# Kernel tuning notes

Measured on AMD Instinct MI355X. Metric: run time of the kernel, lower is better.

Reference implementation:

```python
import jax, jax.numpy as jnp
import numpy as np

B, H, KVH, D, HID = 32, 32, 8, 128, 4096
TPB, MB = 64, 32            # tokens per block, max blocks per seq
NB = B * MB                 # cache pool blocks
S = MB * TPB                # max context = 2048
BASE = 10000.0


def setup_inputs() -> dict:
    key = jax.random.key(0)
    ks = jax.random.split(key, 10)
    ri = lambda k, sh: jax.random.randint(k, sh, -127, 128, dtype=jnp.int8)
    ru = lambda k, sh: jax.random.uniform(k, sh, minval=0.005, maxval=0.02, dtype=jnp.float32)
    return {
        'hidden_q': ri(ks[0], (B, HID)).astype(jnp.int32),
        'hidden_scale': ru(ks[1], (B,)),
        'qkv_w': ri(ks[2], ((H + 2 * KVH) * D, HID)),
        'qkv_wscale': ru(ks[3], ((H + 2 * KVH) * D,)),
        'o_w': ri(ks[4], (HID, H * D)),
        'o_wscale': ru(ks[5], (HID,)),
        'kv_cache': ri(ks[6], (NB, 2, KVH, TPB, D)),
        'kv_scale': ru(ks[7], (NB, 2, KVH, TPB)),
        'block_tables': jnp.arange(NB, dtype=jnp.int32).reshape(B, MB),
        'context_lens': jax.random.randint(ks[8], (B,), 64, S - 1, dtype=jnp.int32),
    }


def _rope_neox(x, pos):
    # x: [B, nH, D], pos: [B] -- GPT-NeoX style rotation on (first half, second half)
    half = D // 2
    inv_freq = jnp.power(BASE, -jnp.arange(half, dtype=jnp.float32) / half)
    ang = pos.astype(jnp.float32)[:, None] * inv_freq[None, :]      # [B, half]
    c = jnp.cos(ang)[:, None, :]
    s = jnp.sin(ang)[:, None, :]
    x1, x2 = x[..., :half], x[..., half:]
    return jnp.concatenate([x1 * c - x2 * s, x2 * c + x1 * s], axis=-1)


def _forward(hidden_q, hidden_scale, qkv_w, qkv_wscale, o_w, o_wscale,
             kv_cache, kv_scale, block_tables, context_lens):
    scaling = D ** -0.5
    # W8A8 qkv GEMM with dynamic per-token input scale + per-channel weight scale
    qkv = (hidden_q.astype(jnp.float32) @ qkv_w.T.astype(jnp.float32))
    qkv = qkv * hidden_scale[:, None] * qkv_wscale[None, :]
    q = qkv[:, :H * D].reshape(B, H, D)
    k = qkv[:, H * D:H * D + KVH * D].reshape(B, KVH, D)
    v = qkv[:, H * D + KVH * D:].reshape(B, KVH, D)

    pos = context_lens                      # next-token position per sequence
    q = _rope_neox(q, pos)
    k = _rope_neox(k, pos)

    # INT8-quantize new k/v per (token, kv_head) and write into paged cache
    k_s = jnp.maximum(jnp.max(jnp.abs(k), axis=-1), 1e-6) / 127.0   # [B, KVH]
    v_s = jnp.maximum(jnp.max(jnp.abs(v), axis=-1), 1e-6) / 127.0
    k_q = jnp.clip(jnp.round(k / k_s[..., None]), -127, 127).astype(kv_cache.dtype)
    v_q = jnp.clip(jnp.round(v / v_s[..., None]), -127, 127).astype(kv_cache.dtype)
    blk = jnp.take_along_axis(block_tables, (pos // TPB)[:, None], axis=1)[:, 0]  # [B]
    slot = pos % TPB
    hi = jnp.arange(KVH)[None, :]
    kv_cache = kv_cache.at[blk[:, None], 0, hi, slot[:, None]].set(k_q)
    kv_cache = kv_cache.at[blk[:, None], 1, hi, slot[:, None]].set(v_q)
    kv_scale = kv_scale.at[blk[:, None], 0, hi, slot[:, None]].set(k_s)
    kv_scale = kv_scale.at[blk[:, None], 1, hi, slot[:, None]].set(v_s)

    # gather paged blocks per sequence and dequantize
    cb = kv_cache[block_tables]                 # [B, MB, 2, KVH, TPB, D] int8
    sb = kv_scale[block_tables]                 # [B, MB, 2, KVH, TPB]
    deq = cb.astype(jnp.float32) * sb[..., None]
    K = deq[:, :, 0].transpose(0, 2, 1, 3, 4).reshape(B, KVH, S, D)
    V = deq[:, :, 1].transpose(0, 2, 1, 3, 4).reshape(B, KVH, S, D)

    # GQA single-query attention over context length (inclusive of new token)
    G = H // KVH
    qg = q.reshape(B, KVH, G, D)
    scores = jnp.einsum('bgqd,bgsd->bgqs', qg, K) * scaling
    valid = jnp.arange(S)[None, :] <= pos[:, None]                  # [B, S]
    scores = jnp.where(valid[:, None, None, :], scores, -jnp.inf)
    probs = jax.nn.softmax(scores, axis=-1)
    attn = jnp.einsum('bgqs,bgsd->bgqd', probs, V).reshape(B, H * D)

    # invoke_quant: per-token dynamic INT8 requant, then W8A8 o_proj
    a_s = jnp.maximum(jnp.max(jnp.abs(attn), axis=-1), 1e-6) / 127.0
    attn_q = jnp.clip(jnp.round(attn / a_s[:, None]), -127, 127)
    out = (attn_q @ o_w.T.astype(jnp.float32)) * a_s[:, None] * o_wscale[None, :]
    return out


def reference(hidden_q, hidden_scale, qkv_w, qkv_wscale, o_w, o_wscale,
              kv_cache, kv_scale, block_tables, context_lens):
    return _forward(hidden_q, hidden_scale, qkv_w, qkv_wscale, o_w, o_wscale,
                    kv_cache, kv_scale, block_tables, context_lens)
```

## Files before the change

kernel.cpp:

```cpp
#include <hip/hip_runtime.h>
#include <math.h>

#define B_    32
#define H_    32
#define KVH_  8
#define D_    128
#define HID_  4096
#define TPB_  64
#define MB_   32
#define G_    4
#define RQKV  6144
#define KS_   16
#define NCH   32
#define SCALING 0.08838834764831845f

typedef __attribute__((ext_vector_type(8))) short short8_t;
typedef __attribute__((ext_vector_type(16))) float f32x16;

__device__ __forceinline__ unsigned int pk2(float lo, float hi) {
  return (__float_as_uint(hi) & 0xffff0000u) | (__float_as_uint(lo) >> 16);
}

__device__ __forceinline__ void gl_lds16(const void* g, void* l) {
  __builtin_amdgcn_global_load_lds((const __attribute__((address_space(1))) void*)g,
                                   (__attribute__((address_space(3))) void*)l, 16, 0, 0);
}

__global__ __launch_bounds__(256) void kprep_x(const int* __restrict__ src, uint4* __restrict__ frag) {
  int gid = blockIdx.x * 256 + threadIdx.x;
  int l = gid & 63, t = gid >> 6;
  int bb = l & 31;
  int k0 = t * 16 + (l >> 5) * 8;
  const int* p = &src[(size_t)bb * HID_ + k0];
  int4 a = *(const int4*)p;
  int4 c = *(const int4*)(p + 4);
  uint4 o;
  o.x = pk2((float)a.x, (float)a.y);
  o.y = pk2((float)a.z, (float)a.w);
  o.z = pk2((float)c.x, (float)c.y);
  o.w = pk2((float)c.z, (float)c.w);
  frag[gid] = o;
}

__global__ __launch_bounds__(256) void kgemm_mfma(const int* __restrict__ W, const uint4* __restrict__ xf,
                                                  float* __restrict__ Yp, int R) {
  __shared__ __align__(16) int wtile[8192];
  int tid = threadIdx.x;
  int wave = tid >> 6, lane = tid & 63;
  int j0 = blockIdx.x * 128;
  int row = lane & 31, hi = lane >> 5;
  int kbase = blockIdx.y * 256;
  uint4 bw[16];
#pragma unroll
  for (int t = 0; t < 16; t++) bw[t] = xf[(size_t)((kbase >> 4) + t) * 64 + lane];
  f32x16 acc;
#pragma unroll
  for (int i = 0; i < 16; i++) acc[i] = 0.f;
  int ldsrow = wave * 32 + row;
  int rsw = ldsrow & 7;
  for (int ss = 0; ss < 4; ss++) {
#pragma unroll
    for (int n = 0; n < 8; n++) {
      int f = n * 4096 + tid * 16;
      int r = f >> 8;
      int sl = (f >> 4) & 15;
      const int* gsrc = W + (size_t)(j0 + r) * HID_ + kbase + ss * 64 + ((sl ^ (r & 7)) << 2);
      gl_lds16(gsrc, (char*)wtile + f);
    }
    __syncthreads();
#pragma unroll
    for (int t = 0; t < 4; t++) {
      int s0 = 4 * t + 2 * hi;
      int4 wa = *(const int4*)&wtile[ldsrow * 64 + ((s0 ^ rsw) << 2)];
      int4 wb = *(const int4*)&wtile[ldsrow * 64 + (((s0 + 1) ^ rsw) << 2)];
      uint4 aw;
      aw.x = pk2((float)wa.x, (float)wa.y);
      aw.y = pk2((float)wa.z, (float)wa.w);
      aw.z = pk2((float)wb.x, (float)wb.y);
      aw.w = pk2((float)wb.z, (float)wb.w);
      acc = __builtin_amdgcn_mfma_f32_32x32x16_bf16(__builtin_bit_cast(short8_t, aw),
                                                    __builtin_bit_cast(short8_t, bw[ss * 4 + t]),
                                                    acc, 0, 0, 0);
    }
    __syncthreads();
  }
  int jw = j0 + wave * 32;
#pragma unroll
  for (int r = 0; r < 16; r++) {
    int rowout = (r & 3) + 8 * (r >> 2) + 4 * hi;
    Yp[((size_t)blockIdx.y * R + jw + rowout) * 32 + (lane & 31)] = acc[r];
  }
}

__global__ __launch_bounds__(256) void kred(const float* __restrict__ Yp, const float* __restrict__ sb,
                                            const float* __restrict__ sj, float* __restrict__ outT, int R) {
  int tid = threadIdx.x;
  int j0 = blockIdx.x * 32;
  __shared__ float lds[32 * 33];
  float acc[4] = {0.f, 0.f, 0.f, 0.f};
  for (int ks = 0; ks < KS_; ks++) {
    const float* p = &Yp[(size_t)ks * R * 32 + j0 * 32];
#pragma unroll
    for (int e = 0; e < 4; e++) acc[e] += p[e * 256 + tid];
  }
#pragma unroll
  for (int e = 0; e < 4; e++) {
    int f = e * 256 + tid;
    int jl = f >> 5, b = f & 31;
    lds[b * 33 + jl] = acc[e];
  }
  __syncthreads();
#pragma unroll
  for (int e = 0; e < 4; e++) {
    int f = e * 256 + tid;
    int b = f >> 5, jl = f & 31;
    outT[(size_t)b * R + j0 + jl] = lds[b * 33 + jl] * sb[b] * sj[j0 + jl];
  }
}

__global__ __launch_bounds__(128) void kpost_qkv(const float* __restrict__ YsT, const int* __restrict__ ctx,
                                                 float* __restrict__ qrope, int* __restrict__ kqf,
                                                 int* __restrict__ vqf, float* __restrict__ ksf,
                                                 float* __restrict__ vsf) {
  int r = blockIdx.x;
  int b = blockIdx.y;
  int d = threadIdx.x;
  float v = YsT[(size_t)b * RQKV + r * 128 + d];
  __shared__ float x[128];
  __shared__ float red[2];
  x[d] = v;
  __syncthreads();
  int pos = ctx[b];
  float val;
  if (r < 40) {
    int i = d & 63;
    float f = powf(10000.f, -(float)i * (1.f / 64.f));
    float ang = (float)pos * f;
    float sv, cv;
    sincosf(ang, &sv, &cv);
    float xa = x[i], xb = x[i + 64];
    val = (d < 64) ? (xa * cv - xb * sv) : (xb * cv + xa * sv);
  } else {
    val = v;
  }
  if (r < 32) { qrope[((size_t)b * H_ + r) * D_ + d] = val; return; }
  float a = fabsf(val);
#pragma unroll
  for (int off = 32; off; off >>= 1) a = fmaxf(a, __shfl_xor(a, off));
  if ((d & 63) == 0) red[d >> 6] = a;
  __syncthreads();
  float mx = fmaxf(red[0], red[1]);
  float sc = fmaxf(mx, 1e-6f) * (1.f / 127.f);
  float qv = rintf(val / sc);
  qv = fminf(fmaxf(qv, -127.f), 127.f);
  int kvh = (r - 32) & 7;
  if (r < 40) {
    kqf[((size_t)b * KVH_ + kvh) * D_ + d] = (int)qv;
    if (d == 0) ksf[b * KVH_ + kvh] = sc;
  } else {
    vqf[((size_t)b * KVH_ + kvh) * D_ + d] = (int)qv;
    if (d == 0) vsf[b * KVH_ + kvh] = sc;
  }
}

__global__ __launch_bounds__(256) void kattn(const int* __restrict__ kvc, const float* __restrict__ kvs,
                                             const int* __restrict__ btab, const int* __restrict__ ctx,
                                             const float* __restrict__ qrope, const int* __restrict__ kqf,
                                             const float* __restrict__ ksf,
                                             const int* __restrict__ vqf, const float* __restrict__ vsf,
                                             float* __restrict__ pm, float* __restrict__ pl,
                                             float* __restrict__ pacc) {
  int cb = blockIdx.x, kvh = blockIdx.y, b = blockIdx.z;
  int tid = threadIdx.x;
  int pos = ctx[b];
  size_t pbase = ((size_t)(b * KVH_ + kvh) * NCH + cb) * G_;
  if (cb * 64 > pos) {
    if (tid < 4) { pm[pbase + tid] = -1e30f; pl[pbase + tid] = 0.f; }
    return;
  }
  __shared__ __align__(16) float qlds[512];
  __shared__ float sls[4][64];
  __shared__ __align__(16) float pls4[64][4];
  __shared__ float pvred[8][516];
  int blk = btab[b * MB_ + cb];
  int freshT = pos - cb * 64;
  const int* kpan = &kvc[(((size_t)(blk * 2 + 0) * KVH_ + kvh) * TPB_) * D_];
  const int* vpan = &kvc[(((size_t)(blk * 2 + 1) * KVH_ + kvh) * TPB_) * D_];

  for (int i = tid; i < 512; i += 256) {
    int sw = i ^ (((i >> 5) & 3) << 2);
    qlds[sw] = qrope[((size_t)b * H_ + kvh * G_) * D_ + i];
  }
  __syncthreads();

  {
    int t = tid >> 2, c = tid & 3;
    const int* krow = kpan + t * 128 + c * 32;
    float kv[32];
#pragma unroll
    for (int i = 0; i < 8; i++) {
      int4 k4 = *(const int4*)&krow[i * 4];
      kv[i * 4 + 0] = (float)k4.x;
      kv[i * 4 + 1] = (float)k4.y;
      kv[i * 4 + 2] = (float)k4.z;
      kv[i * 4 + 3] = (float)k4.w;
    }
    float ksc = kvs[((size_t)(blk * 2 + 0) * KVH_ + kvh) * TPB_ + t] * SCALING;
#pragma unroll
    for (int g = 0; g < 4; g++) {
      int base = g * 128 + c * 32;
      float dot = 0.f;
#pragma unroll
      for (int i = 0; i < 8; i++) {
        float4 q4 = *(const float4*)&qlds[(base + i * 4) ^ (c << 2)];
        dot += kv[i * 4 + 0] * q4.x + kv[i * 4 + 1] * q4.y +
               kv[i * 4 + 2] * q4.z + kv[i * 4 + 3] * q4.w;
      }
      dot += __shfl_xor(dot, 1);
      dot += __shfl_xor(dot, 2);
      if (c == 0) sls[g][t] = dot * ksc;
    }
  }
  __syncthreads();

  {
    int g = tid >> 6, t = tid & 63;
    int s = cb * 64 + t;
    float sc = sls[g][t];
    if (freshT >= 0 && freshT < 64) {
      const int* kk = &kqf[(size_t)(b * KVH_ + kvh) * D_];
      float q1 = qlds[(g * 128 + t) ^ (((t >> 5) & 3) << 2)];
      float q2 = qlds[(g * 128 + 64 + t) ^ ((((t >> 5) + 2) & 3) << 2)];
      float dotf = q1 * (float)kk[t] + q2 * (float)kk[t + 64];
#pragma unroll
      for (int off = 32; off; off >>= 1) dotf += __shfl_xor(dotf, off);
      if (t == freshT) sc = dotf * ksf[b * KVH_ + kvh] * SCALING;
    }
    if (s > pos) sc = -1e30f;
    float m = sc;
#pragma unroll
    for (int off = 32; off; off >>= 1) m = fmaxf(m, __shfl_xor(m, off));
    float p = (s <= pos) ? expf(sc - m) : 0.f;
    float l = p;
#pragma unroll
    for (int off = 32; off; off >>= 1) l += __shfl_xor(l, off);
    if (t == 0) { pm[pbase + g] = m; pl[pbase + g] = l; }
    float vsc = (s == pos) ? vsf[b * KVH_ + kvh]
                           : kvs[((size_t)(blk * 2 + 1) * KVH_ + kvh) * TPB_ + t];
    pls4[t][g] = p * vsc;
  }
  __syncthreads();

  {
    int dq = tid & 31, tg = tid >> 5;
    const int* vb = vpan + dq * 4;
    const int* vfr = vqf + (size_t)(b * KVH_ + kvh) * D_ + dq * 4;
    float a00 = 0.f, a01 = 0.f, a02 = 0.f, a03 = 0.f;
    float a10 = 0.f, a11 = 0.f, a12 = 0.f, a13 = 0.f;
    float a20 = 0.f, a21 = 0.f, a22 = 0.f, a23 = 0.f;
    float a30 = 0.f, a31 = 0.f, a32 = 0.f, a33 = 0.f;
#pragma unroll
    for (int j = 0; j < 8; j++) {
      int tt = tg * 8 + j;
      const int* vr = (tt == freshT) ? vfr : (vb + tt * 128);
      int4 v4 = *(const int4*)vr;
      float4 pp = *(const float4*)&pls4[tt][0];
      float v0 = (float)v4.x, v1 = (float)v4.y, v2 = (float)v4.z, v3 = (float)v4.w;
      a00 = fmaf(pp.x, v0, a00); a01 = fmaf(pp.x, v1, a01); a02 = fmaf(pp.x, v2, a02); a03 = fmaf(pp.x, v3, a03);
      a10 = fmaf(pp.y, v0, a10); a11 = fmaf(pp.y, v1, a11); a12 = fmaf(pp.y, v2, a12); a13 = fmaf(pp.y, v3, a13);
      a20 = fmaf(pp.z, v0, a20); a21 = fmaf(pp.z, v1, a21); a22 = fmaf(pp.z, v2, a22); a23 = fmaf(pp.z, v3, a23);
      a30 = fmaf(pp.w, v0, a30); a31 = fmaf(pp.w, v1, a31); a32 = fmaf(pp.w, v2, a32); a33 = fmaf(pp.w, v3, a33);
    }
    *(float4*)&pvred[tg][0 * 128 + dq * 4] = make_float4(a00, a01, a02, a03);
    *(float4*)&pvred[tg][1 * 128 + dq * 4] = make_float4(a10, a11, a12, a13);
    *(float4*)&pvred[tg][2 * 128 + dq * 4] = make_float4(a20, a21, a22, a23);
    *(float4*)&pvred[tg][3 * 128 + dq * 4] = make_float4(a30, a31, a32, a33);
  }
  __syncthreads();

  {
#pragma unroll
    for (int rr = 0; rr < 2; rr++) {
      int idx = rr * 256 + tid;
      float s = pvred[0][idx] + pvred[1][idx] + pvred[2][idx] + pvred[3][idx] +
                pvred[4][idx] + pvred[5][idx] + pvred[6][idx] + pvred[7][idx];
      pacc[pbase * D_ + idx] = s;
    }
  }
}

__global__ __launch_bounds__(256) void kcomb1(const float* __restrict__ pm, const float* __restrict__ pl,
                                              const float* __restrict__ pacc, float* __restrict__ attnB,
                                              float* __restrict__ amaxp) {
  int sl = blockIdx.x, b = blockIdx.y;
  int tid = threadIdx.x;
  __shared__ float wch[32][32];
  __shared__ float invL[32];
  __shared__ float rbuf[4];
  if (tid < 32) {
    int kvh = tid >> 2, g = tid & 3;
    float M = -1e30f;
    float m[NCH];
#pragma unroll
    for (int ch = 0; ch < NCH; ch++) {
      m[ch] = pm[((size_t)(b * KVH_ + kvh) * NCH + ch) * G_ + g];
      M = fmaxf(M, m[ch]);
    }
    float L = 0.f;
#pragma unroll
    for (int ch = 0; ch < NCH; ch++) {
      float w = expf(m[ch] - M);
      wch[tid][ch] = w;
      L += pl[((size_t)(b * KVH_ + kvh) * NCH + ch) * G_ + g] * w;
    }
    invL[tid] = 1.f / L;
  }
  __syncthreads();
  float amax = 0.f;
#pragma unroll
  for (int rep = 0; rep < 2; rep++) {
    int j = sl * 512 + rep * 256 + tid;
    int h = j >> 7, d = j & 127;
    int kvh = h >> 2, g = h & 3;
    int hh = kvh * 4 + g;
    float v = 0.f;
#pragma unroll 8
    for (int ch = 0; ch < NCH; ch++) {
      float w = wch[hh][ch];
      if (w != 0.f)
        v += pacc[(((size_t)(b * KVH_ + kvh) * NCH + ch) * G_ + g) * D_ + d] * w;
    }
    v *= invL[hh];
    attnB[(size_t)b * (H_ * D_) + j] = v;
    amax = fmaxf(amax, fabsf(v));
  }
#pragma unroll
  for (int off = 32; off; off >>= 1) amax = fmaxf(amax, __shfl_xor(amax, off));
  if ((tid & 63) == 0) rbuf[tid >> 6] = amax;
  __syncthreads();
  if (tid == 0)
    amaxp[b * 8 + sl] = fmaxf(fmaxf(rbuf[0], rbuf[1]), fmaxf(rbuf[2], rbuf[3]));
}

__global__ __launch_bounds__(256) void kcomb2(const float* __restrict__ attnB, const float* __restrict__ amaxp,
                                              uint4* __restrict__ frag, float* __restrict__ asb) {
  int gid = blockIdx.x * 256 + threadIdx.x;
  int l = gid & 63, t = gid >> 6;
  int bb = l & 31;
  int k0 = t * 16 + (l >> 5) * 8;
  float amax = 0.f;
#pragma unroll
  for (int sl = 0; sl < 8; sl++) amax = fmaxf(amax, amaxp[bb * 8 + sl]);
  float as = fmaxf(amax, 1e-6f) * (1.f / 127.f);
  float inv = 1.f / as;
  if (gid < 32) asb[gid] = as;
  const float* src = &attnB[(size_t)bb * (H_ * D_) + k0];
  float4 s0 = *(const float4*)src;
  float4 s1 = *(const float4*)(src + 4);
  float v[8];
  v[0] = s0.x; v[1] = s0.y; v[2] = s0.z; v[3] = s0.w;
  v[4] = s1.x; v[5] = s1.y; v[6] = s1.z; v[7] = s1.w;
#pragma unroll
  for (int e = 0; e < 8; e++) {
    float q = rintf(v[e] * inv);
    v[e] = fminf(fmaxf(q, -127.f), 127.f);
  }
  uint4 o;
  o.x = pk2(v[0], v[1]);
  o.y = pk2(v[2], v[3]);
  o.z = pk2(v[4], v[5]);
  o.w = pk2(v[6], v[7]);
  frag[gid] = o;
}

extern "C" void kernel_launch(void* const* d_in, const int* in_sizes, int n_in,
                              void* d_out, int out_size, void* d_ws, size_t ws_size,
                              hipStream_t stream) {
  const int*   hq    = (const int*)d_in[0];
  const float* hs    = (const float*)d_in[1];
  const int*   qkvw  = (const int*)d_in[2];
  const float* qkvws = (const float*)d_in[3];
  const int*   ow    = (const int*)d_in[4];
  const float* owsc  = (const float*)d_in[5];
  const int*   kvc   = (const int*)d_in[6];
  const float* kvs   = (const float*)d_in[7];
  const int*   btab  = (const int*)d_in[8];
  const int*   ctx   = (const int*)d_in[9];
  float* out = (float*)d_out;

  char* ws = (char*)d_ws;
  uint4* xf    = (uint4*)(ws);
  uint4* af    = (uint4*)(ws + 262144);
  float* Yp    = (float*)(ws + 524288);
  float* YsT   = (float*)(ws + 13107200);
  float* qrope = (float*)(ws + 13893632);
  int*   kqf   = (int*)  (ws + 14417920);
  int*   vqf   = (int*)  (ws + 14548992);
  float* ksf   = (float*)(ws + 14680064);
  float* vsf   = (float*)(ws + 14681088);
  float* pm    = (float*)(ws + 14686208);
  float* pl    = (float*)(ws + 14817280);
  float* pacc  = (float*)(ws + 14948352);
  float* attnB = (float*)(ws + 31725568);
  float* amaxp = (float*)(ws + 32249856);
  float* asb   = (float*)(ws + 32250880);

  kprep_x<<<64, 256, 0, stream>>>(hq, xf);
  kgemm_mfma<<<dim3(RQKV / 128, KS_), 256, 0, stream>>>(qkvw, xf, Yp, RQKV);
  kred<<<RQKV / 32, 256, 0, stream>>>(Yp, hs, qkvws, YsT, RQKV);
  kpost_qkv<<<dim3(48, 32), 128, 0, stream>>>(YsT, ctx, qrope, kqf, vqf, ksf, vsf);
  kattn<<<dim3(NCH, KVH_, B_), 256, 0, stream>>>(kvc, kvs, btab, ctx, qrope, kqf, ksf, vqf, vsf, pm, pl, pacc);
  kcomb1<<<dim3(8, B_), 256, 0, stream>>>(pm, pl, pacc, attnB, amaxp);
  kcomb2<<<64, 256, 0, stream>>>(attnB, amaxp, af, asb);
  kgemm_mfma<<<dim3(HID_ / 128, KS_), 256, 0, stream>>>(ow, af, Yp, HID_);
  kred<<<HID_ / 32, 256, 0, stream>>>(Yp, asb, owsc, out, HID_);
}
```

Baseline: 161.4 us.

## Fuse RoPE and fresh K/V quantization into attention kernel, remove kpost_qkv

Removes the separate kpost_qkv launch. Each attention block now computes RoPE on its query heads directly from the QKV GEMM output. Only the block holding the new token quantizes the fresh K/V, keeping them in shared memory instead of global scratch. The PV stage is also reorganized to 64 d-pairs by 4 token groups with int2 loads, halving the cross-group reduction buffer. This saves a launch and its global round-trip, but every active attention block now recomputes the sincos/powf work for its query heads.

```diff
diff --git a/kernel.cpp b/kernel.cpp
--- a/kernel.cpp
+++ b/kernel.cpp
@@ -118,56 +118,9 @@
   }
 }
 
-__global__ __launch_bounds__(128) void kpost_qkv(const float* __restrict__ YsT, const int* __restrict__ ctx,
-                                                 float* __restrict__ qrope, int* __restrict__ kqf,
-                                                 int* __restrict__ vqf, float* __restrict__ ksf,
-                                                 float* __restrict__ vsf) {
-  int r = blockIdx.x;
-  int b = blockIdx.y;
-  int d = threadIdx.x;
-  float v = YsT[(size_t)b * RQKV + r * 128 + d];
-  __shared__ float x[128];
-  __shared__ float red[2];
-  x[d] = v;
-  __syncthreads();
-  int pos = ctx[b];
-  float val;
-  if (r < 40) {
-    int i = d & 63;
-    float f = powf(10000.f, -(float)i * (1.f / 64.f));
-    float ang = (float)pos * f;
-    float sv, cv;
-    sincosf(ang, &sv, &cv);
-    float xa = x[i], xb = x[i + 64];
-    val = (d < 64) ? (xa * cv - xb * sv) : (xb * cv + xa * sv);
-  } else {
-    val = v;
-  }
-  if (r < 32) { qrope[((size_t)b * H_ + r) * D_ + d] = val; return; }
-  float a = fabsf(val);
-#pragma unroll
-  for (int off = 32; off; off >>= 1) a = fmaxf(a, __shfl_xor(a, off));
-  if ((d & 63) == 0) red[d >> 6] = a;
-  __syncthreads();
-  float mx = fmaxf(red[0], red[1]);
-  float sc = fmaxf(mx, 1e-6f) * (1.f / 127.f);
-  float qv = rintf(val / sc);
-  qv = fminf(fmaxf(qv, -127.f), 127.f);
-  int kvh = (r - 32) & 7;
-  if (r < 40) {
-    kqf[((size_t)b * KVH_ + kvh) * D_ + d] = (int)qv;
-    if (d == 0) ksf[b * KVH_ + kvh] = sc;
-  } else {
-    vqf[((size_t)b * KVH_ + kvh) * D_ + d] = (int)qv;
-    if (d == 0) vsf[b * KVH_ + kvh] = sc;
-  }
-}
-
 __global__ __launch_bounds__(256) void kattn(const int* __restrict__ kvc, const float* __restrict__ kvs,
                                              const int* __restrict__ btab, const int* __restrict__ ctx,
-                                             const float* __restrict__ qrope, const int* __restrict__ kqf,
-                                             const float* __restrict__ ksf,
-                                             const int* __restrict__ vqf, const float* __restrict__ vsf,
+                                             const float* __restrict__ YsT,
                                              float* __restrict__ pm, float* __restrict__ pl,
                                              float* __restrict__ pacc) {
   int cb = blockIdx.x, kvh = blockIdx.y, b = blockIdx.z;
@@ -181,17 +134,58 @@
   __shared__ __align__(16) float qlds[512];
   __shared__ float sls[4][64];
   __shared__ __align__(16) float pls4[64][4];
-  __shared__ float pvred[8][516];
+  __shared__ float kfl[128], vfl[128];
+  __shared__ float red[4];
+  __shared__ __align__(16) float pvred[4][516];
   int blk = btab[b * MB_ + cb];
   int freshT = pos - cb * 64;
+  bool hasfresh = (freshT >= 0 && freshT < 64);
   const int* kpan = &kvc[(((size_t)(blk * 2 + 0) * KVH_ + kvh) * TPB_) * D_];
   const int* vpan = &kvc[(((size_t)(blk * 2 + 1) * KVH_ + kvh) * TPB_) * D_];
-
-  for (int i = tid; i < 512; i += 256) {
-    int sw = i ^ (((i >> 5) & 3) << 2);
-    qlds[sw] = qrope[((size_t)b * H_ + kvh * G_) * D_ + i];
-  }
-  __syncthreads();
+  const float* ys = YsT + (size_t)b * RQKV;
+  float pf = (float)pos;
+
+#pragma unroll
+  for (int r = 0; r < 2; r++) {
+    int e = r * 256 + tid;
+    int hl = e >> 7, d = e & 127, i = d & 63;
+    float f = powf(10000.f, -(float)i * (1.f / 64.f));
+    float sv, cv;
+    sincosf(pf * f, &sv, &cv);
+    int base = (kvh * G_ + hl) * 128;
+    float xa = ys[base + i], xb = ys[base + i + 64];
+    float val = (d < 64) ? (xa * cv - xb * sv) : (xb * cv + xa * sv);
+    qlds[e ^ (((e >> 5) & 3) << 2)] = val;
+  }
+  float fval = 0.f;
+  if (hasfresh) {
+    int d = tid & 127, i = d & 63;
+    int isv = tid >> 7;
+    if (isv == 0) {
+      float f = powf(10000.f, -(float)i * (1.f / 64.f));
+      float sv, cv;
+      sincosf(pf * f, &sv, &cv);
+      int base = 4096 + kvh * 128;
+      float xa = ys[base + i], xb = ys[base + i + 64];
+      fval = (d < 64) ? (xa * cv - xb * sv) : (xb * cv + xa * sv);
+    } else {
+      fval = ys[4096 + 1024 + kvh * 128 + d];
+    }
+    float a = fabsf(fval);
+#pragma unroll
+    for (int off = 32; off; off >>= 1) a = fmaxf(a, __shfl_xor(a, off));
+    if ((tid & 63) == 0) red[tid >> 6] = a;
+  }
+  __syncthreads();
+  if (hasfresh) {
+    int isv = tid >> 7;
+    float mx = fmaxf(red[isv * 2], red[isv * 2 + 1]);
+    float sc = fmaxf(mx, 1e-6f) * (1.f / 127.f);
+    float qv = rintf(fval / sc);
+    qv = fminf(fmaxf(qv, -127.f), 127.f);
+    if (isv == 0) kfl[tid & 127] = qv;
+    else vfl[tid & 127] = qv;
+  }
 
   {
     int t = tid >> 2, c = tid & 3;
@@ -227,14 +221,14 @@
     int g = tid >> 6, t = tid & 63;
     int s = cb * 64 + t;
     float sc = sls[g][t];
-    if (freshT >= 0 && freshT < 64) {
-      const int* kk = &kqf[(size_t)(b * KVH_ + kvh) * D_];
+    if (hasfresh) {
       float q1 = qlds[(g * 128 + t) ^ (((t >> 5) & 3) << 2)];
       float q2 = qlds[(g * 128 + 64 + t) ^ ((((t >> 5) + 2) & 3) << 2)];
-      float dotf = q1 * (float)kk[t] + q2 * (float)kk[t + 64];
+      float dotf = q1 * kfl[t] + q2 * kfl[t + 64];
 #pragma unroll
       for (int off = 32; off; off >>= 1) dotf += __shfl_xor(dotf, off);
-      if (t == freshT) sc = dotf * ksf[b * KVH_ + kvh] * SCALING;
+      float kscl = fmaxf(fmaxf(red[0], red[1]), 1e-6f) * (1.f / 127.f);
+      if (t == freshT) sc = dotf * kscl * SCALING;
     }
     if (s > pos) sc = -1e30f;
     float m = sc;
@@ -245,47 +239,46 @@
 #pragma unroll
     for (int off = 32; off; off >>= 1) l += __shfl_xor(l, off);
     if (t == 0) { pm[pbase + g] = m; pl[pbase + g] = l; }
-    float vsc = (s == pos) ? vsf[b * KVH_ + kvh]
-                           : kvs[((size_t)(blk * 2 + 1) * KVH_ + kvh) * TPB_ + t];
-    pls4[t][g] = p * vsc;
+    float vscl;
+    if (s == pos) vscl = fmaxf(fmaxf(red[2], red[3]), 1e-6f) * (1.f / 127.f);
+    else vscl = kvs[((size_t)(blk * 2 + 1) * KVH_ + kvh) * TPB_ + t];
+    pls4[t][g] = p * vscl;
   }
   __syncthreads();
 
   {
-    int dq = tid & 31, tg = tid >> 5;
-    const int* vb = vpan + dq * 4;
-    const int* vfr = vqf + (size_t)(b * KVH_ + kvh) * D_ + dq * 4;
-    float a00 = 0.f, a01 = 0.f, a02 = 0.f, a03 = 0.f;
-    float a10 = 0.f, a11 = 0.f, a12 = 0.f, a13 = 0.f;
-    float a20 = 0.f, a21 = 0.f, a22 = 0.f, a23 = 0.f;
-    float a30 = 0.f, a31 = 0.f, a32 = 0.f, a33 = 0.f;
-#pragma unroll
-    for (int j = 0; j < 8; j++) {
-      int tt = tg * 8 + j;
-      const int* vr = (tt == freshT) ? vfr : (vb + tt * 128);
-      int4 v4 = *(const int4*)vr;
+    int dq = tid & 63, tg = tid >> 6;
+    const int* vb = vpan + dq * 2;
+    float a00 = 0.f, a01 = 0.f, a10 = 0.f, a11 = 0.f;
+    float a20 = 0.f, a21 = 0.f, a30 = 0.f, a31 = 0.f;
+#pragma unroll
+    for (int j = 0; j < 16; j++) {
+      int tt = tg * 16 + j;
+      float v0, v1;
+      if (tt == freshT) {
+        v0 = vfl[dq * 2]; v1 = vfl[dq * 2 + 1];
+      } else {
+        int2 vv = *(const int2*)(vb + (size_t)tt * 128);
+        v0 = (float)vv.x; v1 = (float)vv.y;
+      }
       float4 pp = *(const float4*)&pls4[tt][0];
-      float v0 = (float)v4.x, v1 = (float)v4.y, v2 = (float)v4.z, v3 = (float)v4.w;
-      a00 = fmaf(pp.x, v0, a00); a01 = fmaf(pp.x, v1, a01); a02 = fmaf(pp.x, v2, a02); a03 = fmaf(pp.x, v3, a03);
-      a10 = fmaf(pp.y, v0, a10); a11 = fmaf(pp.y, v1, a11); a12 = fmaf(pp.y, v2, a12); a13 = fmaf(pp.y, v3, a13);
-      a20 = fmaf(pp.z, v0, a20); a21 = fmaf(pp.z, v1, a21); a22 = fmaf(pp.z, v2, a22); a23 = fmaf(pp.z, v3, a23);
-      a30 = fmaf(pp.w, v0, a30); a31 = fmaf(pp.w, v1, a31); a32 = fmaf(pp.w, v2, a32); a33 = fmaf(pp.w, v3, a33);
-    }
-    *(float4*)&pvred[tg][0 * 128 + dq * 4] = make_float4(a00, a01, a02, a03);
-    *(float4*)&pvred[tg][1 * 128 + dq * 4] = make_float4(a10, a11, a12, a13);
-    *(float4*)&pvred[tg][2 * 128 + dq * 4] = make_float4(a20, a21, a22, a23);
-    *(float4*)&pvred[tg][3 * 128 + dq * 4] = make_float4(a30, a31, a32, a33);
-  }
-  __syncthreads();
-
-  {
-#pragma unroll
-    for (int rr = 0; rr < 2; rr++) {
-      int idx = rr * 256 + tid;
-      float s = pvred[0][idx] + pvred[1][idx] + pvred[2][idx] + pvred[3][idx] +
-                pvred[4][idx] + pvred[5][idx] + pvred[6][idx] + pvred[7][idx];
-      pacc[pbase * D_ + idx] = s;
-    }
+      a00 = fmaf(pp.x, v0, a00); a01 = fmaf(pp.x, v1, a01);
+      a10 = fmaf(pp.y, v0, a10); a11 = fmaf(pp.y, v1, a11);
+      a20 = fmaf(pp.z, v0, a20); a21 = fmaf(pp.z, v1, a21);
+      a30 = fmaf(pp.w, v0, a30); a31 = fmaf(pp.w, v1, a31);
+    }
+    *(float2*)&pvred[tg][0 * 128 + dq * 2] = make_float2(a00, a01);
+    *(float2*)&pvred[tg][1 * 128 + dq * 2] = make_float2(a10, a11);
+    *(float2*)&pvred[tg][2 * 128 + dq * 2] = make_float2(a20, a21);
+    *(float2*)&pvred[tg][3 * 128 + dq * 2] = make_float2(a30, a31);
+  }
+  __syncthreads();
+
+#pragma unroll
+  for (int rr = 0; rr < 2; rr++) {
+    int idx = rr * 256 + tid;
+    float s = pvred[0][idx] + pvred[1][idx] + pvred[2][idx] + pvred[3][idx];
+    pacc[pbase * D_ + idx] = s;
   }
 }
 
@@ -393,23 +386,17 @@
   uint4* af    = (uint4*)(ws + 262144);
   float* Yp    = (float*)(ws + 524288);
   float* YsT   = (float*)(ws + 13107200);
-  float* qrope = (float*)(ws + 13893632);
-  int*   kqf   = (int*)  (ws + 14417920);
-  int*   vqf   = (int*)  (ws + 14548992);
-  float* ksf   = (float*)(ws + 14680064);
-  float* vsf   = (float*)(ws + 14681088);
-  float* pm    = (float*)(ws + 14686208);
-  float* pl    = (float*)(ws + 14817280);
-  float* pacc  = (float*)(ws + 14948352);
-  float* attnB = (float*)(ws + 31725568);
-  float* amaxp = (float*)(ws + 32249856);
-  float* asb   = (float*)(ws + 32250880);
+  float* pm    = (float*)(ws + 13893632);
+  float* pl    = (float*)(ws + 14024704);
+  float* pacc  = (float*)(ws + 14155776);
+  float* attnB = (float*)(ws + 30932992);
+  float* amaxp = (float*)(ws + 31457280);
+  float* asb   = (float*)(ws + 31458304);
 
   kprep_x<<<64, 256, 0, stream>>>(hq, xf);
   kgemm_mfma<<<dim3(RQKV / 128, KS_), 256, 0, stream>>>(qkvw, xf, Yp, RQKV);
   kred<<<RQKV / 32, 256, 0, stream>>>(Yp, hs, qkvws, YsT, RQKV);
-  kpost_qkv<<<dim3(48, 32), 128, 0, stream>>>(YsT, ctx, qrope, kqf, vqf, ksf, vsf);
-  kattn<<<dim3(NCH, KVH_, B_), 256, 0, stream>>>(kvc, kvs, btab, ctx, qrope, kqf, ksf, vqf, vsf, pm, pl, pacc);
+  kattn<<<dim3(NCH, KVH_, B_), 256, 0, stream>>>(kvc, kvs, btab, ctx, YsT, pm, pl, pacc);
   kcomb1<<<dim3(8, B_), 256, 0, stream>>>(pm, pl, pacc, attnB, amaxp);
   kcomb2<<<64, 256, 0, stream>>>(attnB, amaxp, af, asb);
   kgemm_mfma<<<dim3(HID_ / 128, KS_), 256, 0, stream>>>(ow, af, Yp, HID_);
```

After: 214.4 us. +32.8%, slower.

## Fuse split-K reduction into GEMM via last-block atomic counter

Applied to the files above, without the earlier changes.

Removes the separate kred launches by having each split-K GEMM block increment a per-column-tile atomic counter. The last block to finish reduces all partial sums, applies scales and writes the transposed output. Counters are zeroed in kprep_x. This saves two kernel launches and their gaps, but serializes the reduction onto one block per column tile, which now reduces 128 columns instead of 32.

```diff
diff --git a/kernel.cpp b/kernel.cpp
--- a/kernel.cpp
+++ b/kernel.cpp
@@ -26,8 +26,10 @@
                                    (__attribute__((address_space(3))) void*)l, 16, 0, 0);
 }
 
-__global__ __launch_bounds__(256) void kprep_x(const int* __restrict__ src, uint4* __restrict__ frag) {
+__global__ __launch_bounds__(256) void kprep_x(const int* __restrict__ src, uint4* __restrict__ frag,
+                                               int* __restrict__ cnt) {
   int gid = blockIdx.x * 256 + threadIdx.x;
+  if (gid < 80) cnt[gid] = 0;
   int l = gid & 63, t = gid >> 6;
   int bb = l & 31;
   int k0 = t * 16 + (l >> 5) * 8;
@@ -43,8 +45,11 @@
 }
 
 __global__ __launch_bounds__(256) void kgemm_mfma(const int* __restrict__ W, const uint4* __restrict__ xf,
-                                                  float* __restrict__ Yp, int R) {
+                                                  float* __restrict__ Yp, int R,
+                                                  const float* __restrict__ sb, const float* __restrict__ sj,
+                                                  float* __restrict__ outT, int* __restrict__ cnt) {
   __shared__ __align__(16) int wtile[8192];
+  __shared__ int lastflag;
   int tid = threadIdx.x;
   int wave = tid >> 6, lane = tid & 63;
   int j0 = blockIdx.x * 128;
@@ -90,31 +95,37 @@
     int rowout = (r & 3) + 8 * (r >> 2) + 4 * hi;
     Yp[((size_t)blockIdx.y * R + jw + rowout) * 32 + (lane & 31)] = acc[r];
   }
-}
-
-__global__ __launch_bounds__(256) void kred(const float* __restrict__ Yp, const float* __restrict__ sb,
-                                            const float* __restrict__ sj, float* __restrict__ outT, int R) {
-  int tid = threadIdx.x;
-  int j0 = blockIdx.x * 32;
-  __shared__ float lds[32 * 33];
-  float acc[4] = {0.f, 0.f, 0.f, 0.f};
-  for (int ks = 0; ks < KS_; ks++) {
-    const float* p = &Yp[(size_t)ks * R * 32 + j0 * 32];
-#pragma unroll
-    for (int e = 0; e < 4; e++) acc[e] += p[e * 256 + tid];
-  }
-#pragma unroll
-  for (int e = 0; e < 4; e++) {
-    int f = e * 256 + tid;
-    int jl = f >> 5, b = f & 31;
-    lds[b * 33 + jl] = acc[e];
-  }
-  __syncthreads();
-#pragma unroll
-  for (int e = 0; e < 4; e++) {
-    int f = e * 256 + tid;
-    int b = f >> 5, jl = f & 31;
-    outT[(size_t)b * R + j0 + jl] = lds[b * 33 + jl] * sb[b] * sj[j0 + jl];
+  __threadfence();
+  __syncthreads();
+  if (tid == 0) lastflag = (atomicAdd(&cnt[blockIdx.x], 1) == KS_ - 1) ? 1 : 0;
+  __syncthreads();
+  if (lastflag) {
+    __threadfence();
+    float* tl = (float*)wtile;
+    for (int chunk = 0; chunk < 4; chunk++) {
+      int jc = j0 + chunk * 32;
+      float racc[4] = {0.f, 0.f, 0.f, 0.f};
+      for (int ks = 0; ks < KS_; ks++) {
+        const float* p = &Yp[((size_t)ks * R + jc) * 32];
+#pragma unroll
+        for (int e = 0; e < 4; e++) racc[e] += p[e * 256 + tid];
+      }
+      __syncthreads();
+#pragma unroll
+      for (int e = 0; e < 4; e++) {
+        int f = e * 256 + tid;
+        int jl = f >> 5, bb = f & 31;
+        tl[bb * 33 + jl] = racc[e];
+      }
+      __syncthreads();
+#pragma unroll
+      for (int e = 0; e < 4; e++) {
+        int f = e * 256 + tid;
+        int bb = f >> 5, jl = f & 31;
+        outT[(size_t)bb * R + jc + jl] = tl[bb * 33 + jl] * sb[bb] * sj[jc + jl];
+      }
+      __syncthreads();
+    }
   }
 }
 
@@ -278,14 +289,12 @@
   }
   __syncthreads();
 
-  {
-#pragma unroll
-    for (int rr = 0; rr < 2; rr++) {
-      int idx = rr * 256 + tid;
-      float s = pvred[0][idx] + pvred[1][idx] + pvred[2][idx] + pvred[3][idx] +
-                pvred[4][idx] + pvred[5][idx] + pvred[6][idx] + pvred[7][idx];
-      pacc[pbase * D_ + idx] = s;
-    }
+#pragma unroll
+  for (int rr = 0; rr < 2; rr++) {
+    int idx = rr * 256 + tid;
+    float s = pvred[0][idx] + pvred[1][idx] + pvred[2][idx] + pvred[3][idx] +
+              pvred[4][idx] + pvred[5][idx] + pvred[6][idx] + pvred[7][idx];
+    pacc[pbase * D_ + idx] = s;
   }
 }
 
@@ -398,20 +407,19 @@
   int*   vqf   = (int*)  (ws + 14548992);
   float* ksf   = (float*)(ws + 14680064);
   float* vsf   = (float*)(ws + 14681088);
-  float* pm    = (float*)(ws + 14686208);
-  float* pl    = (float*)(ws + 14817280);
-  float* pacc  = (float*)(ws + 14948352);
-  float* attnB = (float*)(ws + 31725568);
-  float* amaxp = (float*)(ws + 32249856);
-  float* asb   = (float*)(ws + 32250880);
-
-  kprep_x<<<64, 256, 0, stream>>>(hq, xf);
-  kgemm_mfma<<<dim3(RQKV / 128, KS_), 256, 0, stream>>>(qkvw, xf, Yp, RQKV);
-  kred<<<RQKV / 32, 256, 0, stream>>>(Yp, hs, qkvws, YsT, RQKV);
+  float* pm    = (float*)(ws + 14682112);
+  float* pl    = (float*)(ws + 14813184);
+  float* pacc  = (float*)(ws + 14944256);
+  float* attnB = (float*)(ws + 31721472);
+  float* amaxp = (float*)(ws + 32245760);
+  float* asb   = (float*)(ws + 32246784);
+  int*   cnt   = (int*)  (ws + 32246912);
+
+  kprep_x<<<64, 256, 0, stream>>>(hq, xf, cnt);
+  kgemm_mfma<<<dim3(RQKV / 128, KS_), 256, 0, stream>>>(qkvw, xf, Yp, RQKV, hs, qkvws, YsT, cnt);
   kpost_qkv<<<dim3(48, 32), 128, 0, stream>>>(YsT, ctx, qrope, kqf, vqf, ksf, vsf);
   kattn<<<dim3(NCH, KVH_, B_), 256, 0, stream>>>(kvc, kvs, btab, ctx, qrope, kqf, ksf, vqf, vsf, pm, pl, pacc);
   kcomb1<<<dim3(8, B_), 256, 0, stream>>>(pm, pl, pacc, attnB, amaxp);
   kcomb2<<<64, 256, 0, stream>>>(attnB, amaxp, af, asb);
-  kgemm_mfma<<<dim3(HID_ / 128, KS_), 256, 0, stream>>>(ow, af, Yp, HID_);
-  kred<<<HID_ / 32, 256, 0, stream>>>(Yp, asb, owsc, out, HID_);
-}
+  kgemm_mfma<<<dim3(HID_ / 128, KS_), 256, 0, stream>>>(ow, af, Yp, HID_, asb, owsc, out, cnt + 48);
+}
```

Result: slower. 357.4 us (+121.4%).

## Fuse attention split combine and activation requantization into one per-batch kernel

Applied to the files above, without the earlier changes.

Merges the two-stage combine (kcomb1 writing attnB and partial absmax, kcomb2 requantizing) into a single kernel with one 1024-thread block per batch row. The combined attention row stays in shared memory, so the absmax reduction and INT8 fragment packing happen in place. This drops one kernel launch and the global round trip through attnB and amaxp. In exchange the combine runs on only 32 blocks instead of 256, so reading pacc relies on far fewer CUs.

```diff
diff --git a/kernel.cpp b/kernel.cpp
--- a/kernel.cpp
+++ b/kernel.cpp
@@ -278,25 +278,24 @@
   }
   __syncthreads();
 
-  {
-#pragma unroll
-    for (int rr = 0; rr < 2; rr++) {
-      int idx = rr * 256 + tid;
-      float s = pvred[0][idx] + pvred[1][idx] + pvred[2][idx] + pvred[3][idx] +
-                pvred[4][idx] + pvred[5][idx] + pvred[6][idx] + pvred[7][idx];
-      pacc[pbase * D_ + idx] = s;
-    }
-  }
-}
-
-__global__ __launch_bounds__(256) void kcomb1(const float* __restrict__ pm, const float* __restrict__ pl,
-                                              const float* __restrict__ pacc, float* __restrict__ attnB,
-                                              float* __restrict__ amaxp) {
-  int sl = blockIdx.x, b = blockIdx.y;
+#pragma unroll
+  for (int rr = 0; rr < 2; rr++) {
+    int idx = rr * 256 + tid;
+    float s = pvred[0][idx] + pvred[1][idx] + pvred[2][idx] + pvred[3][idx] +
+              pvred[4][idx] + pvred[5][idx] + pvred[6][idx] + pvred[7][idx];
+    pacc[pbase * D_ + idx] = s;
+  }
+}
+
+__global__ __launch_bounds__(1024) void kcomb(const float* __restrict__ pm, const float* __restrict__ pl,
+                                              const float* __restrict__ pacc, uint4* __restrict__ frag,
+                                              float* __restrict__ asb) {
+  int b = blockIdx.x;
   int tid = threadIdx.x;
   __shared__ float wch[32][32];
   __shared__ float invL[32];
-  __shared__ float rbuf[4];
+  __shared__ float vbuf[4096];
+  __shared__ float rbuf[16];
   if (tid < 32) {
     int kvh = tid >> 2, g = tid & 3;
     float M = -1e30f;
@@ -318,8 +317,8 @@
   __syncthreads();
   float amax = 0.f;
 #pragma unroll
-  for (int rep = 0; rep < 2; rep++) {
-    int j = sl * 512 + rep * 256 + tid;
+  for (int rep = 0; rep < 4; rep++) {
+    int j = rep * 1024 + tid;
     int h = j >> 7, d = j & 127;
     int kvh = h >> 2, g = h & 3;
     int hh = kvh * 4 + g;
@@ -331,46 +330,35 @@
         v += pacc[(((size_t)(b * KVH_ + kvh) * NCH + ch) * G_ + g) * D_ + d] * w;
     }
     v *= invL[hh];
-    attnB[(size_t)b * (H_ * D_) + j] = v;
+    vbuf[j] = v;
     amax = fmaxf(amax, fabsf(v));
   }
 #pragma unroll
   for (int off = 32; off; off >>= 1) amax = fmaxf(amax, __shfl_xor(amax, off));
   if ((tid & 63) == 0) rbuf[tid >> 6] = amax;
   __syncthreads();
-  if (tid == 0)
-    amaxp[b * 8 + sl] = fmaxf(fmaxf(rbuf[0], rbuf[1]), fmaxf(rbuf[2], rbuf[3]));
-}
-
-__global__ __launch_bounds__(256) void kcomb2(const float* __restrict__ attnB, const float* __restrict__ amaxp,
-                                              uint4* __restrict__ frag, float* __restrict__ asb) {
-  int gid = blockIdx.x * 256 + threadIdx.x;
-  int l = gid & 63, t = gid >> 6;
-  int bb = l & 31;
-  int k0 = t * 16 + (l >> 5) * 8;
-  float amax = 0.f;
-#pragma unroll
-  for (int sl = 0; sl < 8; sl++) amax = fmaxf(amax, amaxp[bb * 8 + sl]);
+  amax = rbuf[0];
+#pragma unroll
+  for (int i = 1; i < 16; i++) amax = fmaxf(amax, rbuf[i]);
   float as = fmaxf(amax, 1e-6f) * (1.f / 127.f);
   float inv = 1.f / as;
-  if (gid < 32) asb[gid] = as;
-  const float* src = &attnB[(size_t)bb * (H_ * D_) + k0];
-  float4 s0 = *(const float4*)src;
-  float4 s1 = *(const float4*)(src + 4);
-  float v[8];
-  v[0] = s0.x; v[1] = s0.y; v[2] = s0.z; v[3] = s0.w;
-  v[4] = s1.x; v[5] = s1.y; v[6] = s1.z; v[7] = s1.w;
-#pragma unroll
-  for (int e = 0; e < 8; e++) {
-    float q = rintf(v[e] * inv);
-    v[e] = fminf(fmaxf(q, -127.f), 127.f);
-  }
-  uint4 o;
-  o.x = pk2(v[0], v[1]);
-  o.y = pk2(v[2], v[3]);
-  o.z = pk2(v[4], v[5]);
-  o.w = pk2(v[6], v[7]);
-  frag[gid] = o;
+  if (tid == 0) asb[b] = as;
+  if (tid < 512) {
+    int t = tid >> 1, hi = tid & 1;
+    int k0 = t * 16 + hi * 8;
+    float v[8];
+#pragma unroll
+    for (int e = 0; e < 8; e++) {
+      float q = rintf(vbuf[k0 + e] * inv);
+      v[e] = fminf(fmaxf(q, -127.f), 127.f);
+    }
+    uint4 o;
+    o.x = pk2(v[0], v[1]);
+    o.y = pk2(v[2], v[3]);
+    o.z = pk2(v[4], v[5]);
+    o.w = pk2(v[6], v[7]);
+    frag[t * 64 + hi * 32 + b] = o;
+  }
 }
 
 extern "C" void kernel_launch(void* const* d_in, const int* in_sizes, int n_in,
@@ -398,20 +386,17 @@
   int*   vqf   = (int*)  (ws + 14548992);
   float* ksf   = (float*)(ws + 14680064);
   float* vsf   = (float*)(ws + 14681088);
-  float* pm    = (float*)(ws + 14686208);
-  float* pl    = (float*)(ws + 14817280);
-  float* pacc  = (float*)(ws + 14948352);
-  float* attnB = (float*)(ws + 31725568);
-  float* amaxp = (float*)(ws + 32249856);
-  float* asb   = (float*)(ws + 32250880);
+  float* pm    = (float*)(ws + 14682112);
+  float* pl    = (float*)(ws + 14813184);
+  float* pacc  = (float*)(ws + 14944256);
+  float* asb   = (float*)(ws + 31721472);
 
   kprep_x<<<64, 256, 0, stream>>>(hq, xf);
   kgemm_mfma<<<dim3(RQKV / 128, KS_), 256, 0, stream>>>(qkvw, xf, Yp, RQKV);
   kred<<<RQKV / 32, 256, 0, stream>>>(Yp, hs, qkvws, YsT, RQKV);
   kpost_qkv<<<dim3(48, 32), 128, 0, stream>>>(YsT, ctx, qrope, kqf, vqf, ksf, vsf);
   kattn<<<dim3(NCH, KVH_, B_), 256, 0, stream>>>(kvc, kvs, btab, ctx, qrope, kqf, ksf, vqf, vsf, pm, pl, pacc);
-  kcomb1<<<dim3(8, B_), 256, 0, stream>>>(pm, pl, pacc, attnB, amaxp);
-  kcomb2<<<64, 256, 0, stream>>>(attnB, amaxp, af, asb);
+  kcomb<<<B_, 1024, 0, stream>>>(pm, pl, pacc, af, asb);
   kgemm_mfma<<<dim3(HID_ / 128, KS_), 256, 0, stream>>>(ow, af, Yp, HID_);
   kred<<<HID_ / 32, 256, 0, stream>>>(Yp, asb, owsc, out, HID_);
 }
```

Result: slower. 174.4 us (+8.1%).
